# Kernel tuning notes

Hardware: AMD Instinct MI355X
Metric: run time of the kernel (lower is better)

The kernel has to match this reference:

```python
import jax, jax.numpy as jnp
import numpy as np

N_NODES = 50000
N_EDGES = 800000
NODE_IN = 5
EDGE_IN = 1
HID = 64


def setup_inputs() -> dict:
    key = jax.random.key(0)
    ks = jax.random.split(key, 16)
    x = jax.random.normal(ks[0], (N_NODES, NODE_IN), dtype=jnp.float32)
    edge_index = jax.random.randint(ks[1], (2, N_EDGES), 0, N_NODES, dtype=jnp.int32)
    edge_attr = jax.random.normal(ks[2], (N_EDGES, EDGE_IN), dtype=jnp.float32)
    def lin(k, fan_in, fan_out):
        b = 1.0 / np.sqrt(fan_in)
        k1, k2 = jax.random.split(k)
        W = jax.random.uniform(k1, (fan_in, fan_out), minval=-b, maxval=b, dtype=jnp.float32)
        bi = jax.random.uniform(k2, (fan_out,), minval=-b, maxval=b, dtype=jnp.float32)
        return W, bi
    W_ne, b_ne = lin(ks[3], NODE_IN, HID)
    W_ee, b_ee = lin(ks[4], EDGE_IN, HID)
    W_gcn, b_gcn = lin(ks[5], HID, HID)   # PyG GCNConv: lin (no bias) + separate bias
    W1, b1 = lin(ks[6], 3 * HID, HID)
    W2, b2 = lin(ks[7], HID, 1)
    return {"x": x, "edge_index": edge_index, "edge_attr": edge_attr,
            "W_ne": W_ne, "b_ne": b_ne, "W_ee": W_ee, "b_ee": b_ee,
            "W_gcn": W_gcn, "b_gcn": b_gcn, "W1": W1, "b1": b1, "W2": W2, "b2": b2}


def gcn_conv(h, edge_index, W, b):
    # PyG GCNConv: add self-loops, symmetric norm D^-1/2 (A+I) D^-1/2, linear, scatter-add.
    N = h.shape[0]
    src, dst = edge_index[0], edge_index[1]
    loops = jnp.arange(N, dtype=src.dtype)
    row = jnp.concatenate([src, loops])  # message sources
    col = jnp.concatenate([dst, loops])  # message targets
    deg = jax.ops.segment_sum(jnp.ones(col.shape[0], h.dtype), col, num_segments=N)
    dinv = jnp.where(deg > 0, jax.lax.rsqrt(deg), 0.0)
    norm = dinv[row] * dinv[col]          # [E+N]
    ht = h @ W                            # [N, HID]
    msg = ht[row] * norm[:, None]         # gather + scale
    return jax.ops.segment_sum(msg, col, num_segments=N) + b


def reference(x, edge_index, edge_attr, W_ne, b_ne, W_ee, b_ee, W_gcn, b_gcn, W1, b1, W2, b2):
    h = jax.nn.relu(x @ W_ne + b_ne)                    # node encoder
    ef = jax.nn.relu(edge_attr @ W_ee + b_ee)           # edge encoder
    h = gcn_conv(h, edge_index, W_gcn, b_gcn)           # GCN layer
    src, dst = edge_index[0], edge_index[1]
    edge_input = jnp.concatenate([h[src], h[dst], ef], axis=1)  # [E, 3*HID]
    out = jax.nn.relu(edge_input @ W1 + b1) @ W2 + b2   # edge MLP -> [E, 1]
    return out.reshape(-1)
```

## Files before the change

### kernel.cpp

```cpp
#include <hip/hip_runtime.h>

#define NN 50000
#define NE 800000
#define H  64
#define NBKT 196
#define BCAP 8192
#define BIN_CHUNK 2048
#define NBIN (NE + BIN_CHUNK - 1) / BIN_CHUNK
#define CT4N (65 * 37)

typedef __attribute__((ext_vector_type(8))) short bf16x8;
typedef __attribute__((ext_vector_type(4))) float f32x4;

__device__ __forceinline__ unsigned short f2bf(float f) {
  unsigned int u = __builtin_bit_cast(unsigned int, f);
  u += 0x7FFFu + ((u >> 16) & 1u);
  return (unsigned short)(u >> 16);
}
__device__ __forceinline__ float bf2f(unsigned short u) {
  unsigned int v = ((unsigned int)u) << 16;
  return __builtin_bit_cast(float, v);
}

__global__ __launch_bounds__(256) void k_bin(
    const int* __restrict__ ei, unsigned int* __restrict__ gbin,
    int* __restrict__ gcur,
    const float* __restrict__ W1, const float* __restrict__ b1,
    const float* __restrict__ W_ee, const float* __restrict__ b_ee,
    float* __restrict__ thrS, float* __restrict__ cT,
    unsigned short* __restrict__ w1f) {
  const int t = threadIdx.x;

  if (blockIdx.x == NBIN + 1) {
    const int ln = t & 63, q = t >> 6;
    const int l15_ = ln & 15, l4_ = ln >> 4;
#pragma unroll
    for (int f = 0; f < 4; ++f) {
      const int idx = q * 4 + f;
      const int g = idx >> 3;
      const int ct = (idx >> 1) & 3;
      const int c = idx & 1;
#pragma unroll
      for (int j = 0; j < 8; ++j) {
        const int k = g * 64 + c * 32 + l4_ * 8 + j;
        const int hcol = ct * 16 + l15_;
        w1f[(idx * 64 + ln) * 8 + j] = f2bf(W1[k * H + hcol]);
      }
    }
    return;
  }

  if (blockIdx.x == NBIN) {
    __shared__ float swee[64], sbee[64], sth[64];
    __shared__ int skx[64];
    if (t < 64) {
      const float w = W_ee[t], b = b_ee[t];
      swee[t] = w; sbee[t] = b;
      sth[t] = (w != 0.f) ? (-b / w) : __builtin_inff();
      skx[t] = t;
    }
    __syncthreads();
    for (int sz = 2; sz <= 64; sz <<= 1)
      for (int st = sz >> 1; st > 0; st >>= 1) {
        if (t < 64) {
          const int p = t ^ st;
          if (p > t) {
            const bool up = ((t & sz) == 0);
            const float a = sth[t], bb = sth[p];
            if (up ? (a > bb) : (a < bb)) {
              const int ka = skx[t];
              sth[t] = bb; sth[p] = a;
              skx[t] = skx[p]; skx[p] = ka;
            }
          }
        }
        __syncthreads();
      }
    if (t < 64) {
      const int h = t;
      const int l4h = h >> 4, rh = (h & 15) >> 1, sub = h & 1;
      float c1 = 0.f, c0 = b1[h];
      for (int k = 0; k < 64; ++k) {
        const float w = swee[k], b = sbee[k];
        if (w < 0.f || (w == 0.f && b > 0.f)) {
          const float wv1 = W1[(128 + k) * H + h];
          c1 = fmaf(w, wv1, c1);
          c0 = fmaf(b, wv1, c0);
        }
      }
      {
        float* base = cT + (size_t)(0 * 37 + l4h * 9 + rh) * 4;
        base[2 * sub] = c1; base[2 * sub + 1] = c0;
      }
      for (int iv = 1; iv <= 64; ++iv) {
        const int ks = skx[iv - 1];
        const float w = swee[ks];
        const float s = (w > 0.f) ? 1.f : -1.f;
        const float wv1 = W1[(128 + ks) * H + h];
        c1 = fmaf(s * w, wv1, c1);
        c0 = fmaf(s * sbee[ks], wv1, c0);
        float* base = cT + (size_t)(iv * 37 + l4h * 9 + rh) * 4;
        base[2 * sub] = c1; base[2 * sub + 1] = c0;
      }
      thrS[h] = sth[h];
    }
    return;
  }

  __shared__ int hist[NBKT], base[NBKT];
  if (t < NBKT) hist[t] = 0;
  __syncthreads();

  const int e0 = blockIdx.x * BIN_CHUNK;
  int srcv[8], dstv[8], loff[8];
#pragma unroll
  for (int j = 0; j < 8; ++j) {
    const int e = e0 + j * 256 + t;
    if (e < NE) {
      srcv[j] = ei[e];
      dstv[j] = ei[NE + e];
      loff[j] = atomicAdd(&hist[dstv[j] >> 8], 1);
    } else dstv[j] = -1;
  }
  __syncthreads();
  if (t < NBKT) base[t] = atomicAdd(&gcur[t], hist[t]);
  __syncthreads();
#pragma unroll
  for (int j = 0; j < 8; ++j) {
    if (dstv[j] >= 0) {
      const int b = dstv[j] >> 8;
      const int pos = base[b] + loff[j];
      if (pos < BCAP)
        gbin[(size_t)b * BCAP + pos] =
            ((unsigned int)srcv[j] << 8) | (unsigned int)(dstv[j] & 255);
    }
  }
}

__global__ __launch_bounds__(256) void k_pass2(const unsigned int* __restrict__ gbin,
                                               const int* __restrict__ gcur,
                                               unsigned short* __restrict__ gcsr,
                                               int2* __restrict__ rowrange,
                                               float* __restrict__ dinv) {
  __shared__ int hist[256], cur[256], sc[256];
  __shared__ unsigned short lcsr[BCAP];
  const int b = blockIdx.x, t = threadIdx.x;
  const int sz = min(gcur[b], BCAP);
  hist[t] = 0;
  __syncthreads();

  const unsigned int* bb = gbin + (size_t)b * BCAP;
  unsigned int ent[32];
#pragma unroll
  for (int k = 0; k < 32; ++k) {
    const int i = t + k * 256;
    if (i < sz) {
      ent[k] = bb[i];
      atomicAdd(&hist[ent[k] & 255], 1);
    }
  }
  __syncthreads();

  int v = hist[t];
  const int cnt = v;
  sc[t] = v;
  __syncthreads();
#pragma unroll
  for (int off = 1; off < 256; off <<= 1) {
    const int o = (t >= off) ? sc[t - off] : 0;
    __syncthreads();
    v += o;
    sc[t] = v;
    __syncthreads();
  }
  const int ex = v - cnt;
  cur[t] = ex;
  const int d = b * 256 + t;
  if (d < NN) {
    const int beg = b * BCAP + ex;
    rowrange[d] = make_int2(beg, beg + cnt);
    dinv[d] = rsqrtf((float)(cnt + 1));
  }
  __syncthreads();

#pragma unroll
  for (int k = 0; k < 32; ++k) {
    const int i = t + k * 256;
    if (i < sz) {
      const unsigned int en = ent[k];
      const int off = atomicAdd(&cur[en & 255], 1);
      lcsr[off] = (unsigned short)(en >> 8);
    }
  }
  __syncthreads();
  for (int i = t; i < sz; i += 256) gcsr[(size_t)b * BCAP + i] = lcsr[i];
}

__global__ __launch_bounds__(256) void k_node(
    const float* __restrict__ x, const float* __restrict__ W_ne,
    const float* __restrict__ b_ne, const float* __restrict__ W_gcn,
    const float* __restrict__ dinv, unsigned short* __restrict__ htb) {
  __shared__ float sh[4][H];
  const int lane = threadIdx.x & 63;
  const int wv   = threadIdx.x >> 6;
  const int n    = blockIdx.x * 4 + wv;

  float acc = b_ne[lane];
#pragma unroll
  for (int k = 0; k < 5; ++k) acc = fmaf(x[n * 5 + k], W_ne[k * H + lane], acc);
  acc = fmaxf(acc, 0.0f);
  sh[wv][lane] = acc;
  __syncthreads();

  float hv = 0.0f;
#pragma unroll 8
  for (int k = 0; k < H; ++k) hv = fmaf(sh[wv][k], W_gcn[k * H + lane], hv);

  htb[(size_t)n * H + lane] = f2bf(hv * dinv[n]);
}

__global__ __launch_bounds__(256) void k_gather_uv(
    const int2* __restrict__ rowrange, const unsigned short* __restrict__ gcsr,
    const unsigned short* __restrict__ htb, const float* __restrict__ dinv,
    const float* __restrict__ b_gcn, const unsigned short* __restrict__ w1f,
    unsigned short* __restrict__ u, unsigned short* __restrict__ v) {
  __shared__ unsigned short shg[16 * 64];
  const int lane = threadIdx.x & 63;
  const int wv   = threadIdx.x >> 6;
  const int n0   = blockIdx.x * 16;
  const float bg = b_gcn[lane];

#pragma unroll 1
  for (int q = 0; q < 4; ++q) {
    const int nl = wv * 4 + q;
    const int n  = n0 + nl;
    const int2 rr = rowrange[n];
    float sum = bf2f(htb[(size_t)n * H + lane]);
    int i = rr.x;
#pragma unroll 1
    for (; i + 8 <= rr.y; i += 8) {
      const int s0 = gcsr[i],     s1 = gcsr[i + 1];
      const int s2 = gcsr[i + 2], s3 = gcsr[i + 3];
      const int s4 = gcsr[i + 4], s5 = gcsr[i + 5];
      const int s6 = gcsr[i + 6], s7 = gcsr[i + 7];
      const float v0 = bf2f(htb[(size_t)s0 * H + lane]);
      const float v1 = bf2f(htb[(size_t)s1 * H + lane]);
      const float v2 = bf2f(htb[(size_t)s2 * H + lane]);
      const float v3 = bf2f(htb[(size_t)s3 * H + lane]);
      const float v4 = bf2f(htb[(size_t)s4 * H + lane]);
      const float v5 = bf2f(htb[(size_t)s5 * H + lane]);
      const float v6 = bf2f(htb[(size_t)s6 * H + lane]);
      const float v7 = bf2f(htb[(size_t)s7 * H + lane]);
      sum += ((v0 + v1) + (v2 + v3)) + ((v4 + v5) + (v6 + v7));
    }
#pragma unroll 1
    for (; i < rr.y; ++i) sum += bf2f(htb[(size_t)gcsr[i] * H + lane]);

    const float hgv = fmaf(dinv[n], sum, bg);
    shg[((nl * 128 + lane * 2) ^ ((nl & 7) << 4)) >> 1] = f2bf(hgv);
  }
  __syncthreads();

  const int l15 = lane & 15, l4 = lane >> 4;
  const bf16x8 a0 = *(const bf16x8*)(shg + (((l15 * 128 + l4 * 16) ^ ((l15 & 7) << 4)) >> 1));
  const bf16x8 a1 = *(const bf16x8*)(shg + (((l15 * 128 + 64 + l4 * 16) ^ ((l15 & 7) << 4)) >> 1));

  const int ct = wv;
  const bf16x8 bu0 = *(const bf16x8*)(w1f + ((ct * 2 + 0) * 64 + lane) * 8);
  const bf16x8 bu1 = *(const bf16x8*)(w1f + ((ct * 2 + 1) * 64 + lane) * 8);
  const bf16x8 bv0 = *(const bf16x8*)(w1f + ((8 + ct * 2 + 0) * 64 + lane) * 8);
  const bf16x8 bv1 = *(const bf16x8*)(w1f + ((8 + ct * 2 + 1) * 64 + lane) * 8);

  f32x4 au = (f32x4)(0.f), av = (f32x4)(0.f);
  au = __builtin_amdgcn_mfma_f32_16x16x32_bf16(a0, bu0, au, 0, 0, 0);
  au = __builtin_amdgcn_mfma_f32_16x16x32_bf16(a1, bu1, au, 0, 0, 0);
  av = __builtin_amdgcn_mfma_f32_16x16x32_bf16(a0, bv0, av, 0, 0, 0);
  av = __builtin_amdgcn_mfma_f32_16x16x32_bf16(a1, bv1, av, 0, 0, 0);

#pragma unroll
  for (int r = 0; r < 4; ++r) {
    const size_t idx = (size_t)(n0 + l4 * 4 + r) * H + ct * 16 + l15;
    u[idx] = f2bf(au[r]);
    v[idx] = f2bf(av[r]);
  }
}

__device__ __forceinline__ int find_iv(const float* __restrict__ sThr, float ea) {
  int iv = 0;
#pragma unroll
  for (int st = 64; st >= 1; st >>= 1) {
    const int nc = iv + st;
    if (nc <= 64 && sThr[nc - 1] <= ea) iv = nc;
  }
  return iv;
}

__device__ __forceinline__ void edge_compute(
    float ea, uint4 U0, uint4 U1, uint4 V0, uint4 V1,
    const float* __restrict__ sThr, const float4* __restrict__ sCT4,
    const float* __restrict__ w2v, int l4, int lane, float b2v,
    float* __restrict__ out, int obase) {
  const int iv = find_iv(sThr, ea);
  const float4* cp = sCT4 + iv * 37 + l4 * 9;
  const unsigned int ud[8] = {U0.x, U0.y, U0.z, U0.w, U1.x, U1.y, U1.z, U1.w};
  const unsigned int vd[8] = {V0.x, V0.y, V0.z, V0.w, V1.x, V1.y, V1.z, V1.w};
  float p = 0.f;
#pragma unroll
  for (int r = 0; r < 8; ++r) {
    const float4 cc = cp[r];
    const float ulo = __builtin_bit_cast(float, ud[r] << 16);
    const float uhi = __builtin_bit_cast(float, ud[r] & 0xFFFF0000u);
    const float vlo = __builtin_bit_cast(float, vd[r] << 16);
    const float vhi = __builtin_bit_cast(float, vd[r] & 0xFFFF0000u);
    const float z0 = ulo + vlo + fmaf(ea, cc.x, cc.y);
    const float z1 = uhi + vhi + fmaf(ea, cc.z, cc.w);
    p = fmaf(fmaxf(z0, 0.f), w2v[2 * r], p);
    p = fmaf(fmaxf(z1, 0.f), w2v[2 * r + 1], p);
  }
  p += __shfl_xor(p, 16);
  p += __shfl_xor(p, 32);
  if (lane < 16) out[obase + lane] = p + b2v;
}

#define ET 5
__global__ __launch_bounds__(512) void k_edge(
    const int* __restrict__ ei, const float* __restrict__ eattr,
    const unsigned short* __restrict__ u, const unsigned short* __restrict__ v,
    const float* __restrict__ thrS, const float* __restrict__ cT,
    const float* __restrict__ W2, const float* __restrict__ b2,
    float* __restrict__ out) {
  __shared__ float sThr[64];
  __shared__ float4 sCT4[CT4N];

  const int t = threadIdx.x;
  if (t < 64) sThr[t] = thrS[t];
  {
    const float4* g = (const float4*)cT;
    for (int i = t; i < CT4N; i += 512) sCT4[i] = g[i];
  }
  __syncthreads();

  const int lane = t & 63;
  const int wv   = t >> 6;
  const int l15  = lane & 15, l4 = lane >> 4;
  const float b2v = b2[0];

  float w2v[16];
#pragma unroll
  for (int j = 0; j < 16; ++j) w2v[j] = W2[l4 * 16 + j];

  const int tile0 = (blockIdx.x * 8 + wv) * ET;
  int srcA[ET], dstA[ET];
  float eaA[ET];
#pragma unroll
  for (int tt = 0; tt < ET; ++tt) {
    srcA[tt] = ei[(tile0 + tt) * 16 + l15];
    dstA[tt] = ei[NE + (tile0 + tt) * 16 + l15];
    eaA[tt]  = eattr[(tile0 + tt) * 16 + l15];
  }

  uint4 Au0, Au1, Av0, Av1, Bu0, Bu1, Bv0, Bv1;

#define LOADUV(U0, U1, V0, V1, tt) {                               \
    const unsigned short* up = u + (size_t)srcA[tt] * H + l4 * 16; \
    const unsigned short* vp = v + (size_t)dstA[tt] * H + l4 * 16; \
    U0 = *(const uint4*)(up); U1 = *(const uint4*)(up + 8);        \
    V0 = *(const uint4*)(vp); V1 = *(const uint4*)(vp + 8); }

  LOADUV(Au0, Au1, Av0, Av1, 0);
  LOADUV(Bu0, Bu1, Bv0, Bv1, 1);
  edge_compute(eaA[0], Au0, Au1, Av0, Av1, sThr, sCT4, w2v, l4, lane, b2v, out, (tile0 + 0) * 16);
  LOADUV(Au0, Au1, Av0, Av1, 2);
  edge_compute(eaA[1], Bu0, Bu1, Bv0, Bv1, sThr, sCT4, w2v, l4, lane, b2v, out, (tile0 + 1) * 16);
  LOADUV(Bu0, Bu1, Bv0, Bv1, 3);
  edge_compute(eaA[2], Au0, Au1, Av0, Av1, sThr, sCT4, w2v, l4, lane, b2v, out, (tile0 + 2) * 16);
  LOADUV(Au0, Au1, Av0, Av1, 4);
  edge_compute(eaA[3], Bu0, Bu1, Bv0, Bv1, sThr, sCT4, w2v, l4, lane, b2v, out, (tile0 + 3) * 16);
  edge_compute(eaA[4], Au0, Au1, Av0, Av1, sThr, sCT4, w2v, l4, lane, b2v, out, (tile0 + 4) * 16);
#undef LOADUV
}

extern "C" void kernel_launch(void* const* d_in, const int* in_sizes, int n_in,
                              void* d_out, int out_size, void* d_ws, size_t ws_size,
                              hipStream_t stream) {
  const float* x     = (const float*)d_in[0];
  const int*   ei    = (const int*)d_in[1];
  const float* eattr = (const float*)d_in[2];
  const float* W_ne  = (const float*)d_in[3];
  const float* b_ne  = (const float*)d_in[4];
  const float* W_ee  = (const float*)d_in[5];
  const float* b_ee  = (const float*)d_in[6];
  const float* W_gcn = (const float*)d_in[7];
  const float* b_gcn = (const float*)d_in[8];
  const float* W1    = (const float*)d_in[9];
  const float* b1    = (const float*)d_in[10];
  const float* W2    = (const float*)d_in[11];
  const float* b2    = (const float*)d_in[12];
  float* out = (float*)d_out;

  char* ws = (char*)d_ws;
  unsigned short* htb = (unsigned short*)(ws + 0);
  unsigned short* uT  = (unsigned short*)(ws + 6400000);
  unsigned int*   gbin = (unsigned int*)(ws + 12800000);
  unsigned short* vT  = (unsigned short*)(ws + 12800000);
  unsigned short* gcsr = (unsigned short*)(ws + 19222528);
  int2*  rowrange = (int2*)(ws + 22433792);
  float* dinv    = (float*)(ws + 22833792);
  int*   gcur    = (int*)(ws + 23033792);
  float* thrS    = (float*)(ws + 23034592);
  float* cT      = (float*)(ws + 23034848);
  unsigned short* w1f = (unsigned short*)(ws + 23073328);

  hipMemsetAsync(gcur, 0, NBKT * sizeof(int), stream);
  k_bin<<<NBIN + 2, 256, 0, stream>>>(ei, gbin, gcur, W1, b1, W_ee, b_ee, thrS, cT, w1f);
  k_pass2<<<NBKT, 256, 0, stream>>>(gbin, gcur, gcsr, rowrange, dinv);
  k_node<<<NN / 4, 256, 0, stream>>>(x, W_ne, b_ne, W_gcn, dinv, htb);
  k_gather_uv<<<NN / 16, 256, 0, stream>>>(rowrange, gcsr, htb, dinv, b_gcn, w1f, uT, vT);
  k_edge<<<NE / (8 * ET * 16), 512, 0, stream>>>(ei, eattr, uT, vT, thrS, cT, W2, b2, out);
}
```

Before: 148.7 us.

## Fuse node transform into binning and CSR build into gather kernel

Merges the node encoder and GCN linear into extra blocks of the binning kernel. It also folds the per-bucket CSR construction into the gather+MFMA kernel, shrinking buckets to 64 nodes so the CSR stays in shared memory. Degree normalization now comes from a global atomic count, and the source-side dinv is applied during the gather through an extra cnt load and rsqrt per neighbor. This removes two launches and the gcsr/rowrange global round trip. The cost is per-edge global atomics and extra per-neighbor loads.

```diff
diff --git a/kernel.cpp b/kernel.cpp
--- a/kernel.cpp
+++ b/kernel.cpp
@@ -3,10 +3,11 @@
 #define NN 50000
 #define NE 800000
 #define H  64
-#define NBKT 196
-#define BCAP 8192
+#define NBKT 784
+#define BCAP 2048
 #define BIN_CHUNK 2048
-#define NBIN (NE + BIN_CHUNK - 1) / BIN_CHUNK
+#define NBIN ((NE + BIN_CHUNK - 1) / BIN_CHUNK)
+#define NODE_BLKS (NN / 4)
 #define CT4N (65 * 37)
 
 typedef __attribute__((ext_vector_type(8))) short bf16x8;
@@ -24,14 +25,35 @@
 
 __global__ __launch_bounds__(256) void k_bin(
     const int* __restrict__ ei, unsigned int* __restrict__ gbin,
-    int* __restrict__ gcur,
+    int* __restrict__ gcur, int* __restrict__ cnt,
+    const float* __restrict__ x, const float* __restrict__ W_ne,
+    const float* __restrict__ b_ne, const float* __restrict__ W_gcn,
+    unsigned short* __restrict__ htb,
     const float* __restrict__ W1, const float* __restrict__ b1,
     const float* __restrict__ W_ee, const float* __restrict__ b_ee,
     float* __restrict__ thrS, float* __restrict__ cT,
     unsigned short* __restrict__ w1f) {
   const int t = threadIdx.x;
 
-  if (blockIdx.x == NBIN + 1) {
+  if (blockIdx.x < NODE_BLKS) {
+    __shared__ float sh[4][H];
+    const int lane = t & 63;
+    const int wv   = t >> 6;
+    const int n    = blockIdx.x * 4 + wv;
+    float acc = b_ne[lane];
+#pragma unroll
+    for (int k = 0; k < 5; ++k) acc = fmaf(x[n * 5 + k], W_ne[k * H + lane], acc);
+    acc = fmaxf(acc, 0.0f);
+    sh[wv][lane] = acc;
+    __syncthreads();
+    float hv = 0.0f;
+#pragma unroll 8
+    for (int k = 0; k < H; ++k) hv = fmaf(sh[wv][k], W_gcn[k * H + lane], hv);
+    htb[(size_t)n * H + lane] = f2bf(hv);
+    return;
+  }
+
+  if (blockIdx.x == NODE_BLKS + NBIN + 1) {
     const int ln = t & 63, q = t >> 6;
     const int l15_ = ln & 15, l4_ = ln >> 4;
 #pragma unroll
@@ -50,7 +72,7 @@
     return;
   }
 
-  if (blockIdx.x == NBIN) {
+  if (blockIdx.x == NODE_BLKS + NBIN) {
     __shared__ float swee[64], sbee[64], sth[64];
     __shared__ int skx[64];
     if (t < 64) {
@@ -108,10 +130,10 @@
   }
 
   __shared__ int hist[NBKT], base[NBKT];
-  if (t < NBKT) hist[t] = 0;
-  __syncthreads();
-
-  const int e0 = blockIdx.x * BIN_CHUNK;
+  for (int i = t; i < NBKT; i += 256) hist[i] = 0;
+  __syncthreads();
+
+  const int e0 = (blockIdx.x - NODE_BLKS) * BIN_CHUNK;
   int srcv[8], dstv[8], loff[8];
 #pragma unroll
   for (int j = 0; j < 8; ++j) {
@@ -119,169 +141,148 @@
     if (e < NE) {
       srcv[j] = ei[e];
       dstv[j] = ei[NE + e];
-      loff[j] = atomicAdd(&hist[dstv[j] >> 8], 1);
+      loff[j] = atomicAdd(&hist[dstv[j] >> 6], 1);
+      atomicAdd(&cnt[dstv[j]], 1);
     } else dstv[j] = -1;
   }
   __syncthreads();
-  if (t < NBKT) base[t] = atomicAdd(&gcur[t], hist[t]);
+  for (int i = t; i < NBKT; i += 256) base[i] = atomicAdd(&gcur[i], hist[i]);
   __syncthreads();
 #pragma unroll
   for (int j = 0; j < 8; ++j) {
     if (dstv[j] >= 0) {
-      const int b = dstv[j] >> 8;
+      const int b = dstv[j] >> 6;
       const int pos = base[b] + loff[j];
       if (pos < BCAP)
         gbin[(size_t)b * BCAP + pos] =
-            ((unsigned int)srcv[j] << 8) | (unsigned int)(dstv[j] & 255);
-    }
-  }
-}
-
-__global__ __launch_bounds__(256) void k_pass2(const unsigned int* __restrict__ gbin,
-                                               const int* __restrict__ gcur,
-                                               unsigned short* __restrict__ gcsr,
-                                               int2* __restrict__ rowrange,
-                                               float* __restrict__ dinv) {
-  __shared__ int hist[256], cur[256], sc[256];
+            ((unsigned int)srcv[j] << 6) | (unsigned int)(dstv[j] & 63);
+    }
+  }
+}
+
+__global__ __launch_bounds__(256) void k_pg(
+    const unsigned int* __restrict__ gbin, const int* __restrict__ gcur,
+    const int* __restrict__ cnt, const unsigned short* __restrict__ htb,
+    const float* __restrict__ b_gcn, const unsigned short* __restrict__ w1f,
+    unsigned short* __restrict__ u, unsigned short* __restrict__ v) {
+  __shared__ int hist[64], cur[64], sc[64], sbeg[64];
+  __shared__ float sdinv[64];
   __shared__ unsigned short lcsr[BCAP];
+  __shared__ unsigned short shg[16 * 64];
   const int b = blockIdx.x, t = threadIdx.x;
   const int sz = min(gcur[b], BCAP);
-  hist[t] = 0;
+  if (t < 64) hist[t] = 0;
   __syncthreads();
 
   const unsigned int* bb = gbin + (size_t)b * BCAP;
-  unsigned int ent[32];
-#pragma unroll
-  for (int k = 0; k < 32; ++k) {
+  unsigned int ent[8];
+#pragma unroll
+  for (int k = 0; k < 8; ++k) {
     const int i = t + k * 256;
     if (i < sz) {
       ent[k] = bb[i];
-      atomicAdd(&hist[ent[k] & 255], 1);
-    }
-  }
-  __syncthreads();
-
-  int v = hist[t];
-  const int cnt = v;
-  sc[t] = v;
-  __syncthreads();
-#pragma unroll
-  for (int off = 1; off < 256; off <<= 1) {
-    const int o = (t >= off) ? sc[t - off] : 0;
-    __syncthreads();
-    v += o;
-    sc[t] = v;
-    __syncthreads();
-  }
-  const int ex = v - cnt;
-  cur[t] = ex;
-  const int d = b * 256 + t;
-  if (d < NN) {
-    const int beg = b * BCAP + ex;
-    rowrange[d] = make_int2(beg, beg + cnt);
-    dinv[d] = rsqrtf((float)(cnt + 1));
-  }
-  __syncthreads();
-
-#pragma unroll
-  for (int k = 0; k < 32; ++k) {
+      atomicAdd(&hist[ent[k] & 63], 1);
+    }
+  }
+  __syncthreads();
+
+  int vinc = (t < 64) ? hist[t] : 0;
+  if (t < 64) sc[t] = vinc;
+  __syncthreads();
+#pragma unroll
+  for (int off = 1; off < 64; off <<= 1) {
+    const int o = (t >= off && t < 64) ? sc[t - off] : 0;
+    __syncthreads();
+    if (t < 64) { vinc += o; sc[t] = vinc; }
+    __syncthreads();
+  }
+  if (t < 64) {
+    const int c = hist[t];
+    const int ex = vinc - c;
+    cur[t] = ex;
+    sbeg[t] = ex;
+    sdinv[t] = rsqrtf((float)(c + 1));
+  }
+  __syncthreads();
+
+#pragma unroll
+  for (int k = 0; k < 8; ++k) {
     const int i = t + k * 256;
     if (i < sz) {
       const unsigned int en = ent[k];
-      const int off = atomicAdd(&cur[en & 255], 1);
-      lcsr[off] = (unsigned short)(en >> 8);
-    }
-  }
-  __syncthreads();
-  for (int i = t; i < sz; i += 256) gcsr[(size_t)b * BCAP + i] = lcsr[i];
-}
-
-__global__ __launch_bounds__(256) void k_node(
-    const float* __restrict__ x, const float* __restrict__ W_ne,
-    const float* __restrict__ b_ne, const float* __restrict__ W_gcn,
-    const float* __restrict__ dinv, unsigned short* __restrict__ htb) {
-  __shared__ float sh[4][H];
-  const int lane = threadIdx.x & 63;
-  const int wv   = threadIdx.x >> 6;
-  const int n    = blockIdx.x * 4 + wv;
-
-  float acc = b_ne[lane];
-#pragma unroll
-  for (int k = 0; k < 5; ++k) acc = fmaf(x[n * 5 + k], W_ne[k * H + lane], acc);
-  acc = fmaxf(acc, 0.0f);
-  sh[wv][lane] = acc;
-  __syncthreads();
-
-  float hv = 0.0f;
-#pragma unroll 8
-  for (int k = 0; k < H; ++k) hv = fmaf(sh[wv][k], W_gcn[k * H + lane], hv);
-
-  htb[(size_t)n * H + lane] = f2bf(hv * dinv[n]);
-}
-
-__global__ __launch_bounds__(256) void k_gather_uv(
-    const int2* __restrict__ rowrange, const unsigned short* __restrict__ gcsr,
-    const unsigned short* __restrict__ htb, const float* __restrict__ dinv,
-    const float* __restrict__ b_gcn, const unsigned short* __restrict__ w1f,
-    unsigned short* __restrict__ u, unsigned short* __restrict__ v) {
-  __shared__ unsigned short shg[16 * 64];
-  const int lane = threadIdx.x & 63;
-  const int wv   = threadIdx.x >> 6;
-  const int n0   = blockIdx.x * 16;
+      const int off = atomicAdd(&cur[en & 63], 1);
+      lcsr[off] = (unsigned short)(en >> 6);
+    }
+  }
+  __syncthreads();
+
+  const int lane = t & 63, wv = t >> 6;
+  const int l15 = lane & 15, l4 = lane >> 4;
   const float bg = b_gcn[lane];
 
+  const bf16x8 bu0 = *(const bf16x8*)(w1f + ((wv * 2 + 0) * 64 + lane) * 8);
+  const bf16x8 bu1 = *(const bf16x8*)(w1f + ((wv * 2 + 1) * 64 + lane) * 8);
+  const bf16x8 bv0 = *(const bf16x8*)(w1f + ((8 + wv * 2 + 0) * 64 + lane) * 8);
+  const bf16x8 bv1 = *(const bf16x8*)(w1f + ((8 + wv * 2 + 1) * 64 + lane) * 8);
+
 #pragma unroll 1
-  for (int q = 0; q < 4; ++q) {
-    const int nl = wv * 4 + q;
-    const int n  = n0 + nl;
-    const int2 rr = rowrange[n];
-    float sum = bf2f(htb[(size_t)n * H + lane]);
-    int i = rr.x;
+  for (int tt = 0; tt < 4; ++tt) {
 #pragma unroll 1
-    for (; i + 8 <= rr.y; i += 8) {
-      const int s0 = gcsr[i],     s1 = gcsr[i + 1];
-      const int s2 = gcsr[i + 2], s3 = gcsr[i + 3];
-      const int s4 = gcsr[i + 4], s5 = gcsr[i + 5];
-      const int s6 = gcsr[i + 6], s7 = gcsr[i + 7];
-      const float v0 = bf2f(htb[(size_t)s0 * H + lane]);
-      const float v1 = bf2f(htb[(size_t)s1 * H + lane]);
-      const float v2 = bf2f(htb[(size_t)s2 * H + lane]);
-      const float v3 = bf2f(htb[(size_t)s3 * H + lane]);
-      const float v4 = bf2f(htb[(size_t)s4 * H + lane]);
-      const float v5 = bf2f(htb[(size_t)s5 * H + lane]);
-      const float v6 = bf2f(htb[(size_t)s6 * H + lane]);
-      const float v7 = bf2f(htb[(size_t)s7 * H + lane]);
-      sum += ((v0 + v1) + (v2 + v3)) + ((v4 + v5) + (v6 + v7));
-    }
+    for (int q = 0; q < 4; ++q) {
+      const int nl = tt * 16 + wv * 4 + q;
+      const int n = b * 64 + nl;
+      float hgv = 0.f;
+      if (n < NN) {
+        const float dn = sdinv[nl];
+        float sum = bf2f(htb[(size_t)n * H + lane]) * dn;
+        const int beg = sbeg[nl], end = beg + hist[nl];
+        int i = beg;
 #pragma unroll 1
-    for (; i < rr.y; ++i) sum += bf2f(htb[(size_t)gcsr[i] * H + lane]);
-
-    const float hgv = fmaf(dinv[n], sum, bg);
-    shg[((nl * 128 + lane * 2) ^ ((nl & 7) << 4)) >> 1] = f2bf(hgv);
-  }
-  __syncthreads();
-
-  const int l15 = lane & 15, l4 = lane >> 4;
-  const bf16x8 a0 = *(const bf16x8*)(shg + (((l15 * 128 + l4 * 16) ^ ((l15 & 7) << 4)) >> 1));
-  const bf16x8 a1 = *(const bf16x8*)(shg + (((l15 * 128 + 64 + l4 * 16) ^ ((l15 & 7) << 4)) >> 1));
-
-  const int ct = wv;
-  const bf16x8 bu0 = *(const bf16x8*)(w1f + ((ct * 2 + 0) * 64 + lane) * 8);
-  const bf16x8 bu1 = *(const bf16x8*)(w1f + ((ct * 2 + 1) * 64 + lane) * 8);
-  const bf16x8 bv0 = *(const bf16x8*)(w1f + ((8 + ct * 2 + 0) * 64 + lane) * 8);
-  const bf16x8 bv1 = *(const bf16x8*)(w1f + ((8 + ct * 2 + 1) * 64 + lane) * 8);
-
-  f32x4 au = (f32x4)(0.f), av = (f32x4)(0.f);
-  au = __builtin_amdgcn_mfma_f32_16x16x32_bf16(a0, bu0, au, 0, 0, 0);
-  au = __builtin_amdgcn_mfma_f32_16x16x32_bf16(a1, bu1, au, 0, 0, 0);
-  av = __builtin_amdgcn_mfma_f32_16x16x32_bf16(a0, bv0, av, 0, 0, 0);
-  av = __builtin_amdgcn_mfma_f32_16x16x32_bf16(a1, bv1, av, 0, 0, 0);
-
-#pragma unroll
-  for (int r = 0; r < 4; ++r) {
-    const size_t idx = (size_t)(n0 + l4 * 4 + r) * H + ct * 16 + l15;
-    u[idx] = f2bf(au[r]);
-    v[idx] = f2bf(av[r]);
+        for (; i + 4 <= end; i += 4) {
+          const int s0 = lcsr[i],     s1 = lcsr[i + 1];
+          const int s2 = lcsr[i + 2], s3 = lcsr[i + 3];
+          const float d0 = rsqrtf((float)(cnt[s0] + 1));
+          const float d1 = rsqrtf((float)(cnt[s1] + 1));
+          const float d2 = rsqrtf((float)(cnt[s2] + 1));
+          const float d3 = rsqrtf((float)(cnt[s3] + 1));
+          const float v0 = bf2f(htb[(size_t)s0 * H + lane]);
+          const float v1 = bf2f(htb[(size_t)s1 * H + lane]);
+          const float v2 = bf2f(htb[(size_t)s2 * H + lane]);
+          const float v3 = bf2f(htb[(size_t)s3 * H + lane]);
+          sum += (v0 * d0 + v1 * d1) + (v2 * d2 + v3 * d3);
+        }
+#pragma unroll 1
+        for (; i < end; ++i) {
+          const int s = lcsr[i];
+          sum = fmaf(bf2f(htb[(size_t)s * H + lane]),
+                     rsqrtf((float)(cnt[s] + 1)), sum);
+        }
+        hgv = fmaf(dn, sum, bg);
+      }
+      const int rloc = nl & 15;
+      shg[((rloc * 128 + lane * 2) ^ ((rloc & 7) << 4)) >> 1] = f2bf(hgv);
+    }
+    __syncthreads();
+
+    const bf16x8 a0 = *(const bf16x8*)(shg + (((l15 * 128 + l4 * 16) ^ ((l15 & 7) << 4)) >> 1));
+    const bf16x8 a1 = *(const bf16x8*)(shg + (((l15 * 128 + 64 + l4 * 16) ^ ((l15 & 7) << 4)) >> 1));
+
+    f32x4 au = (f32x4)(0.f), av = (f32x4)(0.f);
+    au = __builtin_amdgcn_mfma_f32_16x16x32_bf16(a0, bu0, au, 0, 0, 0);
+    au = __builtin_amdgcn_mfma_f32_16x16x32_bf16(a1, bu1, au, 0, 0, 0);
+    av = __builtin_amdgcn_mfma_f32_16x16x32_bf16(a0, bv0, av, 0, 0, 0);
+    av = __builtin_amdgcn_mfma_f32_16x16x32_bf16(a1, bv1, av, 0, 0, 0);
+
+#pragma unroll
+    for (int r = 0; r < 4; ++r) {
+      const int nw = b * 64 + tt * 16 + l4 * 4 + r;
+      if (nw < NN) {
+        const size_t idx = (size_t)nw * H + wv * 16 + l15;
+        u[idx] = f2bf(au[r]);
+        v[idx] = f2bf(av[r]);
+      }
+    }
+    __syncthreads();
   }
 }
 
@@ -403,18 +404,16 @@
   unsigned short* uT  = (unsigned short*)(ws + 6400000);
   unsigned int*   gbin = (unsigned int*)(ws + 12800000);
   unsigned short* vT  = (unsigned short*)(ws + 12800000);
-  unsigned short* gcsr = (unsigned short*)(ws + 19222528);
-  int2*  rowrange = (int2*)(ws + 22433792);
-  float* dinv    = (float*)(ws + 22833792);
-  int*   gcur    = (int*)(ws + 23033792);
-  float* thrS    = (float*)(ws + 23034592);
-  float* cT      = (float*)(ws + 23034848);
-  unsigned short* w1f = (unsigned short*)(ws + 23073328);
-
-  hipMemsetAsync(gcur, 0, NBKT * sizeof(int), stream);
-  k_bin<<<NBIN + 2, 256, 0, stream>>>(ei, gbin, gcur, W1, b1, W_ee, b_ee, thrS, cT, w1f);
-  k_pass2<<<NBKT, 256, 0, stream>>>(gbin, gcur, gcsr, rowrange, dinv);
-  k_node<<<NN / 4, 256, 0, stream>>>(x, W_ne, b_ne, W_gcn, dinv, htb);
-  k_gather_uv<<<NN / 16, 256, 0, stream>>>(rowrange, gcsr, htb, dinv, b_gcn, w1f, uT, vT);
+  int*   cnt     = (int*)(ws + 19222528);
+  int*   gcur    = (int*)(ws + 19422528);
+  float* thrS    = (float*)(ws + 19425664);
+  float* cT      = (float*)(ws + 19425920);
+  unsigned short* w1f = (unsigned short*)(ws + 19464400);
+
+  hipMemsetAsync(cnt, 0, 200000 + 3136, stream);
+  k_bin<<<NODE_BLKS + NBIN + 2, 256, 0, stream>>>(
+      ei, gbin, gcur, cnt, x, W_ne, b_ne, W_gcn, htb,
+      W1, b1, W_ee, b_ee, thrS, cT, w1f);
+  k_pg<<<NBKT, 256, 0, stream>>>(gbin, gcur, cnt, htb, b_gcn, w1f, uT, vT);
   k_edge<<<NE / (8 * ET * 16), 512, 0, stream>>>(ei, eattr, uT, vT, thrS, cT, W2, b2, out);
 }
```

Result: slower. 172.5 us (+16.0%).
